# Optimization experiments

Hardware: AMD Instinct MI355X
Metric: run time of the kernel (lower is better)

## Reference

```python
import jax, jax.numpy as jnp
import numpy as np

NUM_CLASSES = 80
STRIDES = (8, 16, 32)


def _decode(p, stride):
    # p: [B, 5+C, H, W] raw head -> [B, HW, 5+C] decoded (xy in px, wh=exp*stride)
    B, C, H, W = p.shape
    ys, xs = jnp.meshgrid(jnp.arange(H), jnp.arange(W), indexing='ij')
    grid = jnp.stack([xs, ys], -1).reshape(H * W, 2).astype(p.dtype)
    out = p.reshape(B, C, H * W).transpose(0, 2, 1)
    xy = (out[..., :2] + grid) * stride
    wh = jnp.exp(out[..., 2:4]) * stride
    out = jnp.concatenate([xy, wh, out[..., 4:]], -1)
    es = jnp.full((H * W,), float(stride), p.dtype)
    return out, grid[:, 0], grid[:, 1], es


def _pairwise_iou(gt, pr):
    # gt [G,4] cxcywh, pr [A,4] -> [G,A]
    gt_tl = gt[:, None, :2] - gt[:, None, 2:] * 0.5
    gt_br = gt[:, None, :2] + gt[:, None, 2:] * 0.5
    pr_tl = pr[None, :, :2] - pr[None, :, 2:] * 0.5
    pr_br = pr[None, :, :2] + pr[None, :, 2:] * 0.5
    tl = jnp.maximum(gt_tl, pr_tl)
    br = jnp.minimum(gt_br, pr_br)
    en = jnp.all(tl < br, -1).astype(gt.dtype)
    inter = jnp.prod(br - tl, -1) * en
    a_gt = jnp.prod(gt[:, 2:], -1)[:, None]
    a_pr = jnp.prod(pr[:, 2:], -1)[None, :]
    return inter / (a_gt + a_pr - inter + 1e-16)


def _assign(gt_boxes, gt_cls, bbox, clsp, objp, xg, yg, es):
    # SimOTA assignment for one image (all fixed-shape; non-candidate anchors
    # are masked out via huge cost instead of boolean gather).
    G = gt_boxes.shape[0]
    xc = (xg + 0.5) * es  # [A] anchor centers
    yc = (yg + 0.5) * es
    gl = gt_boxes[:, 0:1] - 0.5 * gt_boxes[:, 2:3]
    gr = gt_boxes[:, 0:1] + 0.5 * gt_boxes[:, 2:3]
    gt_ = gt_boxes[:, 1:2] - 0.5 * gt_boxes[:, 3:4]
    gb = gt_boxes[:, 1:2] + 0.5 * gt_boxes[:, 3:4]
    in_box = (xc[None] > gl) & (xc[None] < gr) & (yc[None] > gt_) & (yc[None] < gb)  # [G,A]
    r = 2.5 * es[None]
    in_ctr = ((xc[None] > gt_boxes[:, 0:1] - r) & (xc[None] < gt_boxes[:, 0:1] + r)
              & (yc[None] > gt_boxes[:, 1:2] - r) & (yc[None] < gt_boxes[:, 1:2] + r))
    fg_cand = jnp.any(in_box, 0) | jnp.any(in_ctr, 0)  # [A]
    in_both = in_box & in_ctr  # [G,A]

    ious = _pairwise_iou(gt_boxes, bbox)  # [G,A]
    ious_m = jnp.where(fg_cand[None, :], ious, 0.0)
    iou_cost = -jnp.log(ious_m + 1e-8)

    # pairwise cls BCE cost: bce(sqrt(sigmoid(cls)*sigmoid(obj)), onehot(gt)).sum(-1)
    p = jnp.sqrt(jax.nn.sigmoid(clsp) * jax.nn.sigmoid(objp[:, None]))  # [A,C]
    lp = jnp.maximum(jnp.log(p), -100.0)
    l1p = jnp.maximum(jnp.log1p(-p), -100.0)
    t = jax.nn.one_hot(gt_cls, NUM_CLASSES, dtype=p.dtype)  # [G,C]
    cls_cost = -(jnp.einsum('ac,gc->ga', lp - l1p, t) + jnp.sum(l1p, -1)[None, :])

    cost = (cls_cost + 3.0 * iou_cost
            + 1e5 * (~in_both).astype(p.dtype)
            + 1e9 * (~fg_cand)[None, :].astype(p.dtype))

    # dynamic-k: k_g = clamp(sum(top10 ious), min=1)
    topk_ious, _ = jax.lax.top_k(ious_m, 10)
    dyn_k = jnp.clip(topk_ious.sum(-1).astype(jnp.int32), 1, None)  # [G]
    rank = jnp.argsort(jnp.argsort(cost, axis=1), axis=1)  # rank of each anchor per gt
    matching = (rank < dyn_k[:, None]) & fg_cand[None, :]  # [G,A]
    # resolve anchors matched to multiple gts: keep min-cost gt
    multi = matching.sum(0) > 1
    best = jnp.argmin(cost, 0)
    matching = jnp.where(multi[None, :], jnp.arange(G)[:, None] == best[None, :], matching)

    fg = jnp.any(matching, 0)  # [A]
    matched_gt = jnp.argmax(matching, 0)  # [A]
    pred_iou = jnp.sum(matching * ious, 0)  # [A]
    matched_cls = gt_cls[matched_gt]
    return fg, matched_gt, pred_iou, matched_cls


def _giou_loss(b, g):
    tl = jnp.maximum(b[..., :2] - b[..., 2:] * 0.5, g[..., :2] - g[..., 2:] * 0.5)
    br = jnp.minimum(b[..., :2] + b[..., 2:] * 0.5, g[..., :2] + g[..., 2:] * 0.5)
    area_b = jnp.prod(b[..., 2:], -1)
    area_g = jnp.prod(g[..., 2:], -1)
    en = jnp.all(tl < br, -1).astype(b.dtype)
    inter = jnp.prod(br - tl, -1) * en
    union = area_b + area_g - inter
    iou = inter / (union + 1e-16)
    ctl = jnp.minimum(b[..., :2] - b[..., 2:] * 0.5, g[..., :2] - g[..., 2:] * 0.5)
    cbr = jnp.maximum(b[..., :2] + b[..., 2:] * 0.5, g[..., :2] + g[..., 2:] * 0.5)
    area_c = jnp.maximum(jnp.prod(cbr - ctl, -1), 1e-16)
    giou = iou - (area_c - union) / area_c
    return 1.0 - jnp.clip(giou, -1.0, 1.0)


def _bce_logits(x, t):
    return jnp.maximum(x, 0.0) - x * t + jnp.log1p(jnp.exp(-jnp.abs(x)))


def _forward(p8, p16, p32, labels):
    outs, xo, yo, eo = [], [], [], []
    for p, s in zip((p8, p16, p32), STRIDES):
        o, x, y, e = _decode(p, s)
        outs.append(o); xo.append(x); yo.append(y); eo.append(e)
    outputs = jnp.concatenate(outs, 1)  # [B, A, 5+C]
    xg = jnp.concatenate(xo); yg = jnp.concatenate(yo); es = jnp.concatenate(eo)

    bbox = outputs[..., :4]
    obj = outputs[..., 4]
    cls = outputs[..., 5:]
    gt_boxes = labels[..., :4]
    gt_cls = labels[..., 4].astype(jnp.int32)

    # assignment runs under no_grad in torch
    det = jax.lax.stop_gradient(outputs)
    fg, matched_gt, pred_iou, matched_cls = jax.vmap(
        lambda gb, gc, o: _assign(gb, gc, o[..., :4], o[..., 5:], o[..., 4], xg, yg, es)
    )(gt_boxes, gt_cls, det)

    fgf = fg.astype(outputs.dtype)  # [B,A]
    reg_t = jnp.take_along_axis(gt_boxes, matched_gt[..., None], axis=1)  # [B,A,4]
    cls_t = (jax.nn.one_hot(matched_cls, NUM_CLASSES, dtype=outputs.dtype)
             * pred_iou[..., None] * fgf[..., None])

    loss_iou = jnp.sum(_giou_loss(bbox, reg_t) * fgf)
    loss_obj = jnp.sum(_bce_logits(obj, fgf))
    loss_cls = jnp.sum(_bce_logits(cls, cls_t) * fgf[..., None])
    num_fg = jnp.maximum(jnp.sum(fgf), 1.0)
    return (5.0 * loss_iou + loss_obj + loss_cls) / num_fg


def setup_inputs() -> dict:
    key = jax.random.key(0)
    k1, k2, k3, k4, k5, k6 = jax.random.split(key, 6)
    B, NGT = 32, 20
    p8 = jax.random.normal(k1, (B, 5 + NUM_CLASSES, 80, 80), dtype=jnp.float32)
    p16 = jax.random.normal(k2, (B, 5 + NUM_CLASSES, 40, 40), dtype=jnp.float32)
    p32 = jax.random.normal(k3, (B, 5 + NUM_CLASSES, 20, 20), dtype=jnp.float32)
    cxy = jax.random.uniform(k4, (B, NGT, 2), dtype=jnp.float32, minval=32.0, maxval=608.0)
    wh = jax.random.uniform(k5, (B, NGT, 2), dtype=jnp.float32, minval=16.0, maxval=128.0)
    cls = jax.random.randint(k6, (B, NGT, 1), 0, NUM_CLASSES).astype(jnp.float32)
    labels = jnp.concatenate([cxy, wh, cls], -1)
    return {"p8": p8, "p16": p16, "p32": p32, "labels": labels}


def reference(p8, p16, p32, labels):
    return _forward(p8, p16, p32, labels)
```

## Files before the change

### kernel.cpp

```cpp
#include <hip/hip_runtime.h>
#include <cstdint>
#include <cstddef>

#define NA 8400
#define NAP 8448
#define NB 32
#define NG 20
#define NCL 80
#define NBLK 33

__device__ __forceinline__ float frcp(float x) { return __builtin_amdgcn_rcpf(x); }
__device__ __forceinline__ float bce0(float x) {
  return fmaxf(x, 0.0f) + __logf(1.0f + __expf(-fabsf(x)));
}

__device__ __forceinline__ void anchor_info(int a, const float* p8, const float* p16,
                                            const float* p32, int b, const float*& base,
                                            int& hw, int& HW, int& xg, int& yg, float& fs) {
  if (a < 6400)      { hw = a;        HW = 6400; xg = hw % 80; yg = hw / 80; fs = 8.f;
                       base = p8  + (size_t)b * 85 * 6400; }
  else if (a < 8000) { hw = a - 6400; HW = 1600; xg = hw % 40; yg = hw / 40; fs = 16.f;
                       base = p16 + (size_t)b * 85 * 1600; }
  else               { hw = a - 8000; HW = 400;  xg = hw % 20; yg = hw / 20; fs = 32.f;
                       base = p32 + (size_t)b * 85 * 400; }
}

__device__ __forceinline__ float iou_raw(float gx, float gy, float gw, float gh, float4 p) {
  float gtlx = gx - gw * 0.5f, gtly = gy - gh * 0.5f;
  float gbrx = gx + gw * 0.5f, gbry = gy + gh * 0.5f;
  float ptlx = p.x - p.z * 0.5f, ptly = p.y - p.w * 0.5f;
  float pbrx = p.x + p.z * 0.5f, pbry = p.y + p.w * 0.5f;
  float tlx = fmaxf(gtlx, ptlx), tly = fmaxf(gtly, ptly);
  float brx = fminf(gbrx, pbrx), bry = fminf(gbry, pbry);
  float inter = ((tlx < brx) && (tly < bry)) ? (brx - tlx) * (bry - tly) : 0.0f;
  float ag = gw * gh, ap = p.z * p.w;
  return inter * frcp(ag + ap - inter + 1e-16f);
}

__device__ __forceinline__ float giou_loss(float4 bb, float gx, float gy, float gw, float gh) {
  float btlx = bb.x - bb.z * 0.5f, btly = bb.y - bb.w * 0.5f;
  float bbrx = bb.x + bb.z * 0.5f, bbry = bb.y + bb.w * 0.5f;
  float gtlx = gx - gw * 0.5f, gtly = gy - gh * 0.5f;
  float gbrx = gx + gw * 0.5f, gbry = gy + gh * 0.5f;
  float tlx = fmaxf(btlx, gtlx), tly = fmaxf(btly, gtly);
  float brx = fminf(bbrx, gbrx), bry = fminf(bbry, gbry);
  float area_b = bb.z * bb.w, area_g = gw * gh;
  float inter = ((tlx < brx) && (tly < bry)) ? (brx - tlx) * (bry - tly) : 0.0f;
  float uni = area_b + area_g - inter;
  float iou = inter / (uni + 1e-16f);
  float ctlx = fminf(btlx, gtlx), ctly = fminf(btly, gtly);
  float cbrx = fmaxf(bbrx, gbrx), cbry = fmaxf(bbry, gbry);
  float area_c = fmaxf((cbrx - ctlx) * (cbry - ctly), 1e-16f);
  float giou = iou - (area_c - uni) / area_c;
  giou = fminf(fmaxf(giou, -1.0f), 1.0f);
  return 1.0f - giou;
}

__device__ __forceinline__ void block_argmin(float& v, int& i, volatile float* s_v,
                                             volatile int* s_i, int tid) {
#pragma unroll
  for (int off = 32; off; off >>= 1) {
    float ov = __shfl_down(v, off, 64);
    int   oi = __shfl_down(i, off, 64);
    if (ov < v || (ov == v && oi < i)) { v = ov; i = oi; }
  }
  if ((tid & 63) == 0) { s_v[tid >> 6] = v; s_i[tid >> 6] = i; }
  __syncthreads();
  v = s_v[0]; i = s_i[0];
#pragma unroll
  for (int w = 1; w < 4; ++w) {
    float ov = s_v[w]; int oi = s_i[w];
    if (ov < v || (ov == v && oi < i)) { v = ov; i = oi; }
  }
}

__global__ __launch_bounds__(256) void k1(const float* __restrict__ p8,
                                          const float* __restrict__ p16,
                                          const float* __restrict__ p32,
                                          const float* __restrict__ labels,
                                          int* __restrict__ n_fg_cnt,
                                          int* __restrict__ fg_list,
                                          unsigned int* __restrict__ am_c,
                                          float4* __restrict__ bbox_c,
                                          float* __restrict__ lso_c,
                                          unsigned int* __restrict__ match_c,
                                          float* __restrict__ blk_obj) {
  __shared__ float s_gt[NG * 4];
  __shared__ unsigned int s_wcnt[4];
  __shared__ float s_part[4];
  __shared__ unsigned int s_base;
  int blk = blockIdx.x, b = blockIdx.y, tid = threadIdx.x, lane = tid & 63, wid = tid >> 6;

  if (tid < NG) {
    s_gt[tid * 4 + 0] = labels[((size_t)b * NG + tid) * 5 + 0];
    s_gt[tid * 4 + 1] = labels[((size_t)b * NG + tid) * 5 + 1];
    s_gt[tid * 4 + 2] = labels[((size_t)b * NG + tid) * 5 + 2];
    s_gt[tid * 4 + 3] = labels[((size_t)b * NG + tid) * 5 + 3];
  }
  __syncthreads();

  int a = blk * 256 + tid;
  match_c[(size_t)b * NAP + a] = 0u;

  bool fg = false;
  unsigned int msk = 0u;
  float bce_obj = 0.0f, obj = 0.0f;
  const float* base = nullptr; int hw = 0, HW = 0, xg = 0, yg = 0; float fs = 8.f;
  if (a < NA) {
    anchor_info(a, p8, p16, p32, b, base, hw, HW, xg, yg, fs);
    obj = base[4 * HW + hw];
    bce_obj = bce0(obj);
    float xc = ((float)xg + 0.5f) * fs;
    float yc = ((float)yg + 0.5f) * fs;
    float r = 2.5f * fs;
#pragma unroll
    for (int g = 0; g < NG; ++g) {
      float gx = s_gt[g * 4 + 0], gy = s_gt[g * 4 + 1];
      float gw = s_gt[g * 4 + 2], gh = s_gt[g * 4 + 3];
      bool inb = (xc > gx - 0.5f * gw) && (xc < gx + 0.5f * gw) &&
                 (yc > gy - 0.5f * gh) && (yc < gy + 0.5f * gh);
      bool inc = (xc > gx - r) && (xc < gx + r) && (yc > gy - r) && (yc < gy + r);
      fg = fg || inb || inc;
      if (inb && inc) msk |= (1u << g);
    }
  }

  unsigned long long bm = __ballot(fg);
#pragma unroll
  for (int off = 32; off; off >>= 1) bce_obj += __shfl_down(bce_obj, off, 64);
  if (lane == 0) { s_wcnt[wid] = (unsigned int)__popcll(bm); s_part[wid] = bce_obj; }
  __syncthreads();
  if (tid == 0) {
    unsigned int cnt = s_wcnt[0] + s_wcnt[1] + s_wcnt[2] + s_wcnt[3];
    s_base = cnt ? (unsigned int)atomicAdd(&n_fg_cnt[b], (int)cnt) : 0u;
    blk_obj[b * NBLK + blk] = s_part[0] + s_part[1] + s_part[2] + s_part[3];
  }
  __syncthreads();

  if (!fg) return;
  unsigned int pos = s_base;
  for (int w = 0; w < wid; ++w) pos += s_wcnt[w];
  pos += (unsigned int)__popcll(bm & ((1ull << lane) - 1ull));
  size_t bo = (size_t)b * NAP;
  int ci = (int)pos;
  fg_list[bo + ci] = a;
  am_c[bo + ci] = msk;

  float v0 = base[hw];
  float v1 = base[HW + hw];
  float v2 = base[2 * HW + hw];
  float v3 = base[3 * HW + hw];
  bbox_c[bo + ci] = make_float4((v0 + (float)xg) * fs, (v1 + (float)yg) * fs,
                                __expf(v2) * fs, __expf(v3) * fs);
  float uo = __logf(1.0f + __expf(-fabsf(obj)));
  lso_c[bo + ci] = fminf(obj, 0.0f) - uo;
}

__global__ __launch_bounds__(256) void k23(const float* __restrict__ p8,
                                           const float* __restrict__ p16,
                                           const float* __restrict__ p32,
                                           const float* __restrict__ labels,
                                           const int* __restrict__ fg_list,
                                           const int* __restrict__ n_fg,
                                           const float* __restrict__ lso_c,
                                           const unsigned int* __restrict__ am_c,
                                           const float4* __restrict__ bbox_c,
                                           float* __restrict__ sb_c,
                                           float* __restrict__ cost_tbl,
                                           float* __restrict__ iou_tbl) {
  __shared__ float s_gt[NG * 4];
  __shared__ int   s_gcls[NG];
  __shared__ float s_sl[8][33];
  __shared__ float s_sb[8][33];
  __shared__ float s_slr[32];
  int b = blockIdx.y, tid = threadIdx.x;
  int part = tid >> 5, cl = tid & 31;

  if (tid < NG) {
    s_gt[tid * 4 + 0] = labels[((size_t)b * NG + tid) * 5 + 0];
    s_gt[tid * 4 + 1] = labels[((size_t)b * NG + tid) * 5 + 1];
    s_gt[tid * 4 + 2] = labels[((size_t)b * NG + tid) * 5 + 2];
    s_gt[tid * 4 + 3] = labels[((size_t)b * NG + tid) * 5 + 3];
    s_gcls[tid] = (int)labels[((size_t)b * NG + tid) * 5 + 4];
  }
  __syncthreads();

  int n = n_fg[b];
  size_t bo = (size_t)b * NAP;

  for (int base_ci = blockIdx.x * 32; base_ci < n; base_ci += gridDim.x * 32) {
    int ci = base_ci + cl;
    bool act = ci < n;
    const float* base = nullptr; int hw = 0, HW = 0, xg, yg; float fs;
    float lso = 0.0f, sl = 0.0f, sb = 0.0f;
    if (act) {
      int a = fg_list[bo + ci];
      lso = lso_c[bo + ci];
      anchor_info(a, p8, p16, p32, b, base, hw, HW, xg, yg, fs);
      const float* cb = base + (size_t)(5 + part * 10) * HW + hw;
      float xs[10];
#pragma unroll
      for (int j = 0; j < 10; ++j) xs[j] = cb[(size_t)j * HW];
#pragma unroll
      for (int j = 0; j < 10; ++j) {
        float x = xs[j];
        float u = __logf(1.0f + __expf(-fabsf(x)));
        sb += fmaxf(x, 0.0f) + u;
        float lsx = fminf(x, 0.0f) - u;
        float lpr = 0.5f * (lsx + lso);
        float p   = __expf(lpr);
        sl += fmaxf(__logf(1.0f - p), -100.0f);
      }
    }
    s_sl[part][cl] = sl;
    s_sb[part][cl] = sb;
    __syncthreads();
    if (tid < 32) {
      float tsl = 0.0f, tsb = 0.0f;
#pragma unroll
      for (int q = 0; q < 8; ++q) { tsl += s_sl[q][tid]; tsb += s_sb[q][tid]; }
      s_slr[tid] = tsl;
      if (base_ci + tid < n) sb_c[bo + base_ci + tid] = tsb;
    }
    __syncthreads();
    if (act) {
      float slr = s_slr[cl];
      unsigned int am = am_c[bo + ci];
      float4 pb = bbox_c[bo + ci];
#pragma unroll
      for (int gg = 0; gg < 3; ++gg) {
        int g = part + (gg << 3);
        if (g < NG) {
          int cg = s_gcls[g];
          float x = base[(size_t)(5 + cg) * HW + hw];
          float u = __logf(1.0f + __expf(-fabsf(x)));
          float lsx = fminf(x, 0.0f) - u;
          float lpr = 0.5f * (lsx + lso);
          float p   = __expf(lpr);
          float l1p = fmaxf(__logf(1.0f - p), -100.0f);
          float wv  = fmaxf(lpr, -100.0f) - l1p;
          float iou = iou_raw(s_gt[g * 4 + 0], s_gt[g * 4 + 1],
                              s_gt[g * 4 + 2], s_gt[g * 4 + 3], pb);
          float cst = -(wv + slr) - 3.0f * __logf(iou + 1e-8f);
          if (!((am >> g) & 1u)) cst += 100000.0f;
          size_t row = ((size_t)b * NG + g) * NAP;
          cost_tbl[row + ci] = cst;
          iou_tbl[row + ci]  = iou;
        }
      }
    }
    __syncthreads();
  }
}

__global__ __launch_bounds__(256) void kBCD(const float* __restrict__ p8,
                                            const float* __restrict__ p16,
                                            const float* __restrict__ p32,
                                            const float* __restrict__ labels,
                                            const float* __restrict__ cost_tbl,
                                            const float* __restrict__ iou_tbl,
                                            const int* __restrict__ n_fg,
                                            unsigned int* __restrict__ match_c,
                                            const int* __restrict__ fg_list,
                                            const float4* __restrict__ bbox_c,
                                            const float* __restrict__ sb_c,
                                            const float* __restrict__ blk_obj,
                                            float* __restrict__ accum,
                                            int* __restrict__ done_g,
                                            int* __restrict__ done_img,
                                            float* __restrict__ out) {
  __shared__ float s_cost[NAP];
  __shared__ float s_wt[4 * 10];
  __shared__ float s_v[4];
  __shared__ int   s_i[4];
  __shared__ int   s_k;
  __shared__ int   s_flag;
  __shared__ float s_gt[NG * 5];
  __shared__ float s_red[16];

  int g = blockIdx.x, b = blockIdx.y, tid = threadIdx.x;
  int lane = tid & 63, wid = tid >> 6;
  int n = n_fg[b];
  size_t bo = (size_t)b * NAP;
  const float* __restrict__ cg = cost_tbl + ((size_t)b * NG + g) * NAP;
  const float* __restrict__ ig = iou_tbl  + ((size_t)b * NG + g) * NAP;

  float t10[10];
#pragma unroll
  for (int j = 0; j < 10; ++j) t10[j] = 0.0f;

  for (int ci = tid; ci < n; ci += 256) {
    float iou = ig[ci];
    float cst = cg[ci];
    if (iou > t10[9]) {
      t10[9] = iou;
#pragma unroll
      for (int q = 9; q > 0; --q) {
        if (t10[q] > t10[q - 1]) { float t = t10[q]; t10[q] = t10[q - 1]; t10[q - 1] = t; }
        else break;
      }
    }
    s_cost[ci] = cst;
  }

  for (int r = 0; r < 10; ++r) {
    float v = t10[0];
    float bv = v;
#pragma unroll
    for (int off = 32; off; off >>= 1) bv = fmaxf(bv, __shfl_down(bv, off, 64));
    bv = __shfl(bv, 0, 64);
    unsigned long long won = __ballot(v == bv);
    if (lane == __ffsll(won) - 1) {
#pragma unroll
      for (int q = 0; q < 9; ++q) t10[q] = t10[q + 1];
      t10[9] = -1.0f;
    }
    if (lane == 0) s_wt[wid * 10 + r] = bv;
  }
  __syncthreads();

  if (tid == 0) {
    int p0 = 0, p1 = 0, p2 = 0, p3 = 0;
    float s = 0.0f;
    for (int r = 0; r < 10; ++r) {
      float v0 = (p0 < 10) ? s_wt[p0]      : -2.0f;
      float v1 = (p1 < 10) ? s_wt[10 + p1] : -2.0f;
      float v2 = (p2 < 10) ? s_wt[20 + p2] : -2.0f;
      float v3 = (p3 < 10) ? s_wt[30 + p3] : -2.0f;
      float m = fmaxf(fmaxf(v0, v1), fmaxf(v2, v3));
      s += m;
      if (m == v0) ++p0; else if (m == v1) ++p1; else if (m == v2) ++p2; else ++p3;
    }
    int k = (int)s;
    if (k < 1) k = 1;
    s_k = k;
  }
  __syncthreads();
  int k = s_k;

  for (int it = 0; it < k; ++it) {
    float bv = 3.4e38f; int bi = NAP;
    for (int ci = tid; ci < n; ci += 256) {
      float v = s_cost[ci];
      if (v < bv || (v == bv && ci < bi)) { bv = v; bi = ci; }
    }
    block_argmin(bv, bi, s_v, s_i, tid);
    if (bv >= 1e8f) break;
    if (tid == 0) {
      atomicOr(&match_c[bo + bi], 1u << g);
      s_cost[bi] = 3.4e38f;
    }
    __syncthreads();
  }

  __syncthreads();
  if (tid == 0) {
    __threadfence();
    s_flag = (atomicAdd(&done_g[b], 1) == NG - 1) ? 1 : 0;
  }
  __syncthreads();
  if (!s_flag) return;

  if (tid < NG * 5) s_gt[tid] = labels[(size_t)b * NG * 5 + tid];
  __syncthreads();

  float li = 0.0f, oe = 0.0f, lc = 0.0f, nf = 0.0f;
  for (int ci = tid; ci < n; ci += 256) {
    unsigned int m = atomicOr(&match_c[bo + ci], 0u);
    if (m == 0u) continue;
    int mg;
    if (m & (m - 1)) {
      float bestc = 3.4e38f; mg = 0;
#pragma unroll 4
      for (int gq = 0; gq < NG; ++gq) {
        float cst = cost_tbl[((size_t)b * NG + gq) * NAP + ci];
        if (cst < bestc) { bestc = cst; mg = gq; }
      }
    } else {
      mg = __ffs(m) - 1;
    }
    int a = fg_list[bo + ci];
    const float* base; int hw, HW, xg, yg; float fs;
    anchor_info(a, p8, p16, p32, b, base, hw, HW, xg, yg, fs);
    float4 pb = bbox_c[bo + ci];
    float gx = s_gt[mg * 5], gy = s_gt[mg * 5 + 1];
    float gw = s_gt[mg * 5 + 2], gh = s_gt[mg * 5 + 3];
    int cgq = (int)s_gt[mg * 5 + 4];
    float piou = iou_tbl[((size_t)b * NG + mg) * NAP + ci];
    li += giou_loss(pb, gx, gy, gw, gh);
    float xcls = base[(size_t)(5 + cgq) * HW + hw];
    lc += sb_c[bo + ci] - xcls * piou;
    oe += base[4 * HW + hw];
    nf += 1.0f;
  }

  float vals[4] = {li, oe, lc, nf};
#pragma unroll
  for (int q = 0; q < 4; ++q) {
#pragma unroll
    for (int off = 32; off; off >>= 1) vals[q] += __shfl_down(vals[q], off, 64);
  }
  if ((tid & 63) == 0) {
    int w = tid >> 6;
    s_red[w * 4 + 0] = vals[0];
    s_red[w * 4 + 1] = vals[1];
    s_red[w * 4 + 2] = vals[2];
    s_red[w * 4 + 3] = vals[3];
  }
  __syncthreads();
  if (tid < 4) {
    const int slot[4] = {0, 2, 3, 4};
    float s = s_red[tid] + s_red[4 + tid] + s_red[8 + tid] + s_red[12 + tid];
    atomicAdd(&accum[slot[tid]], s);
  }

  if (tid == 0) {
    __threadfence();
    s_flag = (atomicAdd(done_img, 1) == NB - 1) ? 1 : 0;
  }
  __syncthreads();
  if (!s_flag) return;

  float s = 0.0f;
  for (int i = tid; i < NB * NBLK; i += 256) s += blk_obj[i];
#pragma unroll
  for (int off = 32; off; off >>= 1) s += __shfl_down(s, off, 64);
  if ((tid & 63) == 0) s_red[tid >> 6] = s;
  __syncthreads();
  if (tid == 0) {
    float obj_base = s_red[0] + s_red[1] + s_red[2] + s_red[3];
    float loss_iou = atomicAdd(&accum[0], 0.0f);
    float oex      = atomicAdd(&accum[2], 0.0f);
    float loss_cls = atomicAdd(&accum[3], 0.0f);
    float num_fg   = atomicAdd(&accum[4], 0.0f);
    float loss_obj = obj_base - oex;
    out[0] = (5.0f * loss_iou + loss_obj + loss_cls) / fmaxf(num_fg, 1.0f);
  }
}

extern "C" void kernel_launch(void* const* d_in, const int* in_sizes, int n_in,
                              void* d_out, int out_size, void* d_ws, size_t ws_size,
                              hipStream_t stream) {
  const float* p8     = (const float*)d_in[0];
  const float* p16    = (const float*)d_in[1];
  const float* p32    = (const float*)d_in[2];
  const float* labels = (const float*)d_in[3];
  float* out = (float*)d_out;

  const size_t BAP = (size_t)NB * NAP;
  char* w = (char*)d_ws;
  float4*       bbox_c   = (float4*)w;
  float*        cost_tbl = (float*)(w + BAP * 16);
  float*        iou_tbl  = cost_tbl + (size_t)NB * NG * NAP;
  char*         w2       = (char*)(iou_tbl + (size_t)NB * NG * NAP);
  int*          fg_list  = (int*)(w2);
  unsigned int* match_c  = (unsigned int*)(w2 + BAP * 4);
  float*        sb_c     = (float*)(w2 + BAP * 8);
  float*        lso_c    = (float*)(w2 + BAP * 12);
  unsigned int* am_c     = (unsigned int*)(w2 + BAP * 16);
  char*         w3       = w2 + BAP * 20;
  int*          n_fg     = (int*)w3;
  float*        accum    = (float*)(w3 + 128);
  int*          done_g   = (int*)(w3 + 256);
  int*          done_img = (int*)(w3 + 384);
  float*        blk_obj  = (float*)(w3 + 512);

  hipMemsetAsync(w3, 0, 512, stream);

  k1<<<dim3(NBLK, NB), dim3(256), 0, stream>>>(p8, p16, p32, labels, n_fg, fg_list, am_c,
                                               bbox_c, lso_c, match_c, blk_obj);
  k23<<<dim3(NBLK, NB), dim3(256), 0, stream>>>(p8, p16, p32, labels, fg_list, n_fg, lso_c,
                                                am_c, bbox_c, sb_c, cost_tbl, iou_tbl);
  kBCD<<<dim3(NG, NB), dim3(256), 0, stream>>>(p8, p16, p32, labels, cost_tbl, iou_tbl,
                                               n_fg, match_c, fg_list, bbox_c, sb_c,
                                               blk_obj, accum, done_g, done_img, out);
}
```

Baseline: 176.1 us.

## Replace iterative block argmin with per-thread top-10 cost lists merged once

Each thread now keeps its ten lowest (cost, index) pairs in registers while streaming the candidates. Each wave pops its ten smallest winners, and one thread does a 4-way merge to pick the k lowest-cost anchors. This removes the shared cost array and the k rounds of full scans plus block-wide reductions and barriers. The early-exit threshold rises from 1e8 to 1e37, so results may change if masked costs sit between those values. The added per-thread sorted lists raise register pressure.

```diff
diff --git a/kernel.cpp b/kernel.cpp
--- a/kernel.cpp
+++ b/kernel.cpp
@@ -54,24 +54,6 @@
   float giou = iou - (area_c - uni) / area_c;
   giou = fminf(fmaxf(giou, -1.0f), 1.0f);
   return 1.0f - giou;
-}
-
-__device__ __forceinline__ void block_argmin(float& v, int& i, volatile float* s_v,
-                                             volatile int* s_i, int tid) {
-#pragma unroll
-  for (int off = 32; off; off >>= 1) {
-    float ov = __shfl_down(v, off, 64);
-    int   oi = __shfl_down(i, off, 64);
-    if (ov < v || (ov == v && oi < i)) { v = ov; i = oi; }
-  }
-  if ((tid & 63) == 0) { s_v[tid >> 6] = v; s_i[tid >> 6] = i; }
-  __syncthreads();
-  v = s_v[0]; i = s_i[0];
-#pragma unroll
-  for (int w = 1; w < 4; ++w) {
-    float ov = s_v[w]; int oi = s_i[w];
-    if (ov < v || (ov == v && oi < i)) { v = ov; i = oi; }
-  }
 }
 
 __global__ __launch_bounds__(256) void k1(const float* __restrict__ p8,
@@ -269,11 +251,9 @@
                                             int* __restrict__ done_g,
                                             int* __restrict__ done_img,
                                             float* __restrict__ out) {
-  __shared__ float s_cost[NAP];
   __shared__ float s_wt[4 * 10];
-  __shared__ float s_v[4];
-  __shared__ int   s_i[4];
-  __shared__ int   s_k;
+  __shared__ float s_wc[4 * 10];
+  __shared__ int   s_wi[4 * 10];
   __shared__ int   s_flag;
   __shared__ float s_gt[NG * 5];
   __shared__ float s_red[16];
@@ -286,8 +266,10 @@
   const float* __restrict__ ig = iou_tbl  + ((size_t)b * NG + g) * NAP;
 
   float t10[10];
-#pragma unroll
-  for (int j = 0; j < 10; ++j) t10[j] = 0.0f;
+  float c10v[10];
+  int   c10i[10];
+#pragma unroll
+  for (int j = 0; j < 10; ++j) { t10[j] = 0.0f; c10v[j] = 3.4e38f; c10i[j] = 0x7fffffff; }
 
   for (int ci = tid; ci < n; ci += 256) {
     float iou = ig[ci];
@@ -300,22 +282,50 @@
         else break;
       }
     }
-    s_cost[ci] = cst;
+    if (cst < c10v[9] || (cst == c10v[9] && ci < c10i[9])) {
+      c10v[9] = cst; c10i[9] = ci;
+#pragma unroll
+      for (int q = 9; q > 0; --q) {
+        if (c10v[q] < c10v[q - 1] ||
+            (c10v[q] == c10v[q - 1] && c10i[q] < c10i[q - 1])) {
+          float tv = c10v[q]; c10v[q] = c10v[q - 1]; c10v[q - 1] = tv;
+          int   ti = c10i[q]; c10i[q] = c10i[q - 1]; c10i[q - 1] = ti;
+        } else break;
+      }
+    }
   }
 
   for (int r = 0; r < 10; ++r) {
     float v = t10[0];
     float bv = v;
-#pragma unroll
-    for (int off = 32; off; off >>= 1) bv = fmaxf(bv, __shfl_down(bv, off, 64));
-    bv = __shfl(bv, 0, 64);
+    float cv = c10v[0]; int cix = c10i[0];
+    float cbv = cv;     int cbi = cix;
+#pragma unroll
+    for (int off = 32; off; off >>= 1) {
+      bv = fmaxf(bv, __shfl_down(bv, off, 64));
+      float ov = __shfl_down(cbv, off, 64);
+      int   oi = __shfl_down(cbi, off, 64);
+      if (ov < cbv || (ov == cbv && oi < cbi)) { cbv = ov; cbi = oi; }
+    }
+    bv  = __shfl(bv, 0, 64);
+    cbv = __shfl(cbv, 0, 64);
+    cbi = __shfl(cbi, 0, 64);
     unsigned long long won = __ballot(v == bv);
     if (lane == __ffsll(won) - 1) {
 #pragma unroll
       for (int q = 0; q < 9; ++q) t10[q] = t10[q + 1];
       t10[9] = -1.0f;
     }
-    if (lane == 0) s_wt[wid * 10 + r] = bv;
+    if (cv == cbv && cix == cbi) {
+#pragma unroll
+      for (int q = 0; q < 9; ++q) { c10v[q] = c10v[q + 1]; c10i[q] = c10i[q + 1]; }
+      c10v[9] = 3.4e38f; c10i[9] = 0x7fffffff;
+    }
+    if (lane == 0) {
+      s_wt[wid * 10 + r] = bv;
+      s_wc[wid * 10 + r] = cbv;
+      s_wi[wid * 10 + r] = cbi;
+    }
   }
   __syncthreads();
 
@@ -333,28 +343,21 @@
     }
     int k = (int)s;
     if (k < 1) k = 1;
-    s_k = k;
-  }
-  __syncthreads();
-  int k = s_k;
-
-  for (int it = 0; it < k; ++it) {
-    float bv = 3.4e38f; int bi = NAP;
-    for (int ci = tid; ci < n; ci += 256) {
-      float v = s_cost[ci];
-      if (v < bv || (v == bv && ci < bi)) { bv = v; bi = ci; }
-    }
-    block_argmin(bv, bi, s_v, s_i, tid);
-    if (bv >= 1e8f) break;
-    if (tid == 0) {
+    int q[4] = {0, 0, 0, 0};
+    for (int it = 0; it < k; ++it) {
+      float bv = 3.3e38f; int bi = 0x7fffffff; int sel = -1;
+#pragma unroll
+      for (int w = 0; w < 4; ++w) {
+        if (q[w] < 10) {
+          float v = s_wc[w * 10 + q[w]];
+          int   i = s_wi[w * 10 + q[w]];
+          if (v < bv || (v == bv && i < bi)) { bv = v; bi = i; sel = w; }
+        }
+      }
+      if (sel < 0 || bv >= 1e37f) break;
       atomicOr(&match_c[bo + bi], 1u << g);
-      s_cost[bi] = 3.4e38f;
-    }
-    __syncthreads();
-  }
-
-  __syncthreads();
-  if (tid == 0) {
+      ++q[sel];
+    }
     __threadfence();
     s_flag = (atomicAdd(&done_g[b], 1) == NG - 1) ? 1 : 0;
   }
@@ -396,9 +399,9 @@
 
   float vals[4] = {li, oe, lc, nf};
 #pragma unroll
-  for (int q = 0; q < 4; ++q) {
-#pragma unroll
-    for (int off = 32; off; off >>= 1) vals[q] += __shfl_down(vals[q], off, 64);
+  for (int q2 = 0; q2 < 4; ++q2) {
+#pragma unroll
+    for (int off = 32; off; off >>= 1) vals[q2] += __shfl_down(vals[q2], off, 64);
   }
   if ((tid & 63) == 0) {
     int w = tid >> 6;
```

Result: slower. 183.5 us (+4.2%).
